# Kernel tuning notes

Measured on AMD Instinct MI355X. Metric: run time of the kernel, lower is better.

## Reference

```python
import jax, jax.numpy as jnp
import numpy as np

N = 16384
F_IN = 256
F_OUT = 256


def setup_inputs() -> dict:
    key = jax.random.key(0)
    k1, k2, k3 = jax.random.split(key, 3)
    x = jax.random.normal(k1, (N, F_IN), dtype=jnp.float32)
    # dense 0/1 adjacency (original masks with adj[j] == 1)
    adj = jax.random.randint(k2, (N, N), 0, 2, dtype=jnp.int32)
    # glorot-uniform init for weight [2F_in, F_out]
    stdv = np.sqrt(6.0 / (2 * F_IN + F_OUT)).astype(np.float32)
    weight = jax.random.uniform(k3, (2 * F_IN, F_OUT), dtype=jnp.float32,
                                minval=-stdv, maxval=stdv)
    bias = jnp.zeros((F_OUT,), dtype=jnp.float32)
    return {"x": x, "adj": adj, "weight": weight, "bias": bias}


def reference(x, adj, weight, bias):
    # Mean over neighbors (adj row == 1): segment-mean expressed as a
    # normalized dense matmul -- equivalent to the per-row boolean-mask mean.
    a = adj.astype(x.dtype)                      # [N, N]
    deg = jnp.sum(a, axis=1, keepdims=True)      # [N, 1]
    x1 = (a @ x) / deg                           # [N, F] neighbor mean
    n_x = jnp.concatenate([x1, x], axis=1)       # [N, 2F]
    return n_x @ weight + bias                   # [N, F_out]
```

## Files before the change

kernel.cpp:

```cpp
#include <hip/hip_runtime.h>
#include <hip/hip_bf16.h>
#include <stdint.h>


typedef short bf16x8 __attribute__((ext_vector_type(8)));
typedef float f32x4  __attribute__((ext_vector_type(4)));

__device__ __forceinline__ uint32_t pack_bf16_rne(float lo, float hi) {
    uint32_t ul = __float_as_uint(lo);
    uint32_t uh = __float_as_uint(hi);
    ul = (ul + 0x7fffu + ((ul >> 16) & 1u)) >> 16;
    uh = (uh + 0x7fffu + ((uh >> 16) & 1u)) >> 16;
    return ul | (uh << 16);
}

__global__ __launch_bounds__(256) void k_transpose_w(const float* __restrict__ w,
                                                     uint16_t* __restrict__ wt) {
    int idx = blockIdx.x * 256 + threadIdx.x;
    int n = idx >> 8;
    int k = idx & 255;
    int row = (n < 256) ? k : (256 + k);
    int col = (n < 256) ? n : (n - 256);
    uint32_t u = __float_as_uint(w[row * 256 + col]);
    u = (u + 0x7fffu + ((u >> 16) & 1u)) >> 16;
    wt[idx] = (uint16_t)u;
}

__global__ __launch_bounds__(256) void k_small_gemm(const float* __restrict__ x,
                                                    const uint16_t* __restrict__ wt,
                                                    const float* __restrict__ bias,
                                                    uint16_t* __restrict__ yTt,
                                                    float* __restrict__ z) {
    __shared__ uint16_t As[128 * 32];
    __shared__ uint16_t Bs[128 * 32];

    const int t  = threadIdx.x;
    const int ct = blockIdx.x;
    const int rt = blockIdx.y;
    const int m0 = rt * 128;
    const int n0 = ct * 128;

    const int lane = t & 63, w = t >> 6;
    const int wr = w >> 1, wc = w & 1;
    const int l15 = lane & 15, quad = lane >> 4;

    f32x4 acc[4][4] = {};

    float4 a_reg[4];
    uint4  b_reg[2];

#pragma unroll
    for (int i = 0; i < 4; ++i) {
        int f4 = t + 256 * i, row = f4 >> 3, c4 = f4 & 7;
        a_reg[i] = *(const float4*)(x + (m0 + row) * 256 + c4 * 4);
    }
#pragma unroll
    for (int i = 0; i < 2; ++i) {
        int u4 = t + 256 * i, n_l = u4 >> 2, part = u4 & 3;
        b_reg[i] = *(const uint4*)(wt + (n0 + n_l) * 256 + part * 8);
    }

    for (int kk = 0; kk < 8; ++kk) {
        __syncthreads();
#pragma unroll
        for (int i = 0; i < 4; ++i) {
            int f4 = t + 256 * i, row = f4 >> 3, c4 = f4 & 7;
            uint2 p;
            p.x = pack_bf16_rne(a_reg[i].x, a_reg[i].y);
            p.y = pack_bf16_rne(a_reg[i].z, a_reg[i].w);
            *(uint2*)(As + row * 32 + c4 * 4) = p;
        }
#pragma unroll
        for (int i = 0; i < 2; ++i) {
            int u4 = t + 256 * i, n_l = u4 >> 2, part = u4 & 3;
            *(uint4*)(Bs + n_l * 32 + part * 8) = b_reg[i];
        }
        if (kk < 7) {
            int k0 = (kk + 1) * 32;
#pragma unroll
            for (int i = 0; i < 4; ++i) {
                int f4 = t + 256 * i, row = f4 >> 3, c4 = f4 & 7;
                a_reg[i] = *(const float4*)(x + (m0 + row) * 256 + k0 + c4 * 4);
            }
#pragma unroll
            for (int i = 0; i < 2; ++i) {
                int u4 = t + 256 * i, n_l = u4 >> 2, part = u4 & 3;
                b_reg[i] = *(const uint4*)(wt + (n0 + n_l) * 256 + k0 + part * 8);
            }
        }
        __syncthreads();

        bf16x8 a_frag[4], b_frag[4];
#pragma unroll
        for (int fr = 0; fr < 4; ++fr)
            a_frag[fr] = *(const bf16x8*)(As + (wr * 64 + fr * 16 + l15) * 32 + quad * 8);
#pragma unroll
        for (int fc = 0; fc < 4; ++fc)
            b_frag[fc] = *(const bf16x8*)(Bs + (wc * 64 + fc * 16 + l15) * 32 + quad * 8);
#pragma unroll
        for (int fr = 0; fr < 4; ++fr)
#pragma unroll
            for (int fc = 0; fc < 4; ++fc)
                acc[fr][fc] = __builtin_amdgcn_mfma_f32_16x16x32_bf16(
                    a_frag[fr], b_frag[fc], acc[fr][fc], 0, 0, 0);
    }

    if (ct < 2) {
#pragma unroll
        for (int fr = 0; fr < 4; ++fr) {
            int m_base = m0 + wr * 64 + fr * 16 + quad * 4;
#pragma unroll
            for (int fc = 0; fc < 4; ++fc) {
                int n_g = n0 + wc * 64 + fc * 16 + l15;
                uint2 pp;
                pp.x = pack_bf16_rne(acc[fr][fc][0], acc[fr][fc][1]);
                pp.y = pack_bf16_rne(acc[fr][fc][2], acc[fr][fc][3]);
                *(uint2*)(yTt + (size_t)(m_base >> 5) * 8192 + n_g * 32 + (m_base & 31)) = pp;
            }
        }
    } else {
#pragma unroll
        for (int fr = 0; fr < 4; ++fr) {
            int m_base = m0 + wr * 64 + fr * 16 + quad * 4;
#pragma unroll
            for (int fc = 0; fc < 4; ++fc) {
                int n_g = (n0 - 256) + wc * 64 + fc * 16 + l15;
                float bv = bias[n_g];
#pragma unroll
                for (int r = 0; r < 4; ++r)
                    z[(size_t)(m_base + r) * 256 + n_g] = acc[fr][fc][r] + bv;
            }
        }
    }
}

#define A_STRIDE 36
#define A_SZ (64 * A_STRIDE)
#define KITER 256

#define STEP(ARD, AWR, KK)                                                      \
  do {                                                                          \
    if ((KK) < KITER - 1) {                                \
      _Pragma("unroll") for (int fc = 0; fc < 4; ++fc)                          \
        bN[fc] = *(const bf16x8*)(pB + fc * 512);                               \
      pB += 8192;                                                               \
    }                                                                           \
    if ((KK) < KITER - 3) {                                   \
      aN = pa4[0]; pa4 += 8;                                                    \
    }                                                                           \
    if ((KK) < KITER - 1) {                           \
      degp += aQ0.x + aQ0.y + aQ0.z + aQ0.w;                                    \
      uint2 pv;                                                                 \
      pv.x = (uint32_t)(aQ0.x | (aQ0.y << 16)) * 0x3F80u;                       \
      pv.y = (uint32_t)(aQ0.z | (aQ0.w << 16)) * 0x3F80u;                       \
      *(uint2*)&As##AWR[a_lds] = pv;                                            \
    }                                                                           \
    {                                                                           \
      bf16x8 af[2];                                                             \
      _Pragma("unroll") for (int fr = 0; fr < 2; ++fr) {                        \
        int row = wr * 32 + fr * 16 + l15;                                      \
        af[fr] = *(const bf16x8*)(As##ARD + row * A_STRIDE + quad * 8);         \
      }                                                                         \
      _Pragma("unroll") for (int fr = 0; fr < 2; ++fr)                          \
        _Pragma("unroll") for (int fc = 0; fc < 4; ++fc)                        \
          acc[fr][fc] = __builtin_amdgcn_mfma_f32_16x16x32_bf16(                \
              af[fr], bC[fc], acc[fr][fc], 0, 0, 0);                            \
    }                                                                           \
    aQ0 = aQ1; aQ1 = aQ2; aQ2 = aN;                                             \
    _Pragma("unroll") for (int fc = 0; fc < 4; ++fc) bC[fc] = bN[fc];           \
    asm volatile("s_waitcnt lgkmcnt(0)\n\ts_barrier" ::: "memory");             \
  } while (0)

__global__ __launch_bounds__(512, 4) void k_big_gemm(const int* __restrict__ adj,
                                                     const uint16_t* __restrict__ yTt,
                                                     float* __restrict__ part,
                                                     int* __restrict__ degw) {
    __shared__ uint16_t As0[A_SZ], As1[A_SZ], As2[A_SZ];

    const int t = threadIdx.x;
    const int id   = blockIdx.x + (int)gridDim.x * blockIdx.y;
    const int xcd  = id & 7, slot = id >> 3;
    const int ky   = xcd >> 2;
    const int m0   = ((xcd & 3) * 64 + slot) * 64;
    const int lane = t & 63, w = t >> 6;
    const int wr = w >> 2, wc = w & 3;
    const int l15 = lane & 15, quad = lane >> 4;

    f32x4 acc[2][4] = {};

    const int a_n = t >> 3, a_c4 = t & 7;
    const int4* pa4 = (const int4*)(adj + (size_t)(m0 + a_n) * 16384 + ky * 8192) + a_c4;
    const int a_lds = a_n * A_STRIDE + a_c4 * 4;

    const uint16_t* pB = yTt + (size_t)(ky * 256) * 8192
                       + (size_t)(wc * 64 + l15) * 32 + quad * 8;

    bf16x8 bC[4], bN[4];
    int4 aQ0, aQ1, aQ2, aN;
    int degp;

    int4 a0 = pa4[0];
    aQ0 = pa4[8];
    aQ1 = pa4[16];
    aQ2 = aQ1;
    aN  = aQ1;
    pa4 += 24;
#pragma unroll
    for (int fc = 0; fc < 4; ++fc) bN[fc] = *(const bf16x8*)(pB + fc * 512);
    pB += 8192;
#pragma unroll
    for (int fc = 0; fc < 4; ++fc) bC[fc] = bN[fc];

    degp = a0.x + a0.y + a0.z + a0.w;
    {
        uint2 pv;
        pv.x = (uint32_t)(a0.x | (a0.y << 16)) * 0x3F80u;
        pv.y = (uint32_t)(a0.z | (a0.w << 16)) * 0x3F80u;
        *(uint2*)&As0[a_lds] = pv;
    }
    asm volatile("s_waitcnt lgkmcnt(0)\n\ts_barrier" ::: "memory");

    for (int kk = 0; kk < KITER - 4; kk += 3) {
        STEP(0, 1, kk);
        STEP(1, 2, kk + 1);
        STEP(2, 0, kk + 2);
    }
    STEP(0, 1, 252);
    STEP(1, 2, 253);
    STEP(2, 0, 254);
    STEP(0, 1, 255);

    degp += __shfl_down(degp, 4);
    degp += __shfl_down(degp, 2);
    degp += __shfl_down(degp, 1);
    if ((t & 7) == 0) degw[ky * 16384 + m0 + a_n] = degp;

    float* pc = part + (size_t)ky * 16384 * 256;
#pragma unroll
    for (int fr = 0; fr < 2; ++fr) {
#pragma unroll
        for (int r = 0; r < 4; ++r) {
            int m_l = wr * 32 + fr * 16 + quad * 4 + r;
            size_t mrow = (size_t)(m0 + m_l) * 256;
#pragma unroll
            for (int fc = 0; fc < 4; ++fc) {
                int n_g = wc * 64 + fc * 16 + l15;
                pc[mrow + n_g] = acc[fr][fc][r];
            }
        }
    }
}

__global__ __launch_bounds__(256) void k_reduce(const float* __restrict__ part,
                                                const int* __restrict__ degw,
                                                const float* __restrict__ z,
                                                float* __restrict__ out) {
    int i4 = blockIdx.x * 256 + threadIdx.x;
    int m = i4 >> 6;
    float4 p0 = ((const float4*)part)[i4];
    float4 p1 = ((const float4*)part)[i4 + 16384 * 64];
    float4 zz = ((const float4*)z)[i4];
    float inv = 1.0f / (float)(degw[m] + degw[16384 + m]);
    float4 o;
    o.x = (p0.x + p1.x) * inv + zz.x;
    o.y = (p0.y + p1.y) * inv + zz.y;
    o.z = (p0.z + p1.z) * inv + zz.z;
    o.w = (p0.w + p1.w) * inv + zz.w;
    ((float4*)out)[i4] = o;
}

extern "C" void kernel_launch(void* const* d_in, const int* in_sizes, int n_in,
                              void* d_out, int out_size, void* d_ws, size_t ws_size,
                              hipStream_t stream) {
    const float* x      = (const float*)d_in[0];
    const int*   adj    = (const int*)d_in[1];
    const float* weight = (const float*)d_in[2];
    const float* bias   = (const float*)d_in[3];
    float* out = (float*)d_out;

    char* wsb = (char*)d_ws;
    uint16_t* wt   = (uint16_t*)(wsb);
    uint16_t* yTt  = (uint16_t*)(wsb + 262144);
    float*    z    = (float*)(wsb + 262144 + 8388608);
    float*    partb= (float*)(wsb + 262144 + 8388608 + 16777216);
    int*      degw = (int*)(wsb + 262144 + 8388608 + 16777216 + 33554432);

    k_transpose_w<<<512, 256, 0, stream>>>(weight, wt);
    k_small_gemm<<<dim3(4, 128), 256, 0, stream>>>(x, wt, bias, yTt, z);
    k_big_gemm<<<dim3(256, 2), 512, 0, stream>>>(adj, yTt, partb, degw);
    k_reduce<<<4096, 256, 0, stream>>>(partb, degw, z, out);
}
```

Measured before the change: 1.494 ms.

## Stage B tiles via direct global-to-LDS loads and split K three ways

The big adjacency GEMM now loads the yT operand straight into LDS with global_load_lds and reads it back through XOR-swizzled fragments, replacing per-thread register prefetch. The K split grows from 2 to 3 (171/171/170 tiles), giving 768 blocks, and the XCD-aware block remapping is dropped. The triple-buffered A staging becomes double-buffered, and the kernel adds nontemporal loads and stores, s_setprio around the MFMAs, and a higher occupancy hint. The reduce kernel now sums three partials and degree counts, which costs an extra 16MB partial write and read.

```diff
diff --git a/kernel.cpp b/kernel.cpp
--- a/kernel.cpp
+++ b/kernel.cpp
@@ -5,6 +5,7 @@
 
 typedef short bf16x8 __attribute__((ext_vector_type(8)));
 typedef float f32x4  __attribute__((ext_vector_type(4)));
+typedef int   i32x4  __attribute__((ext_vector_type(4)));
 
 __device__ __forceinline__ uint32_t pack_bf16_rne(float lo, float hi) {
     uint32_t ul = __float_as_uint(lo);
@@ -12,6 +13,12 @@
     ul = (ul + 0x7fffu + ((ul >> 16) & 1u)) >> 16;
     uh = (uh + 0x7fffu + ((uh >> 16) & 1u)) >> 16;
     return ul | (uh << 16);
+}
+
+__device__ __forceinline__ void gld_lds16(const uint16_t* g, uint16_t* l) {
+    __builtin_amdgcn_global_load_lds(
+        (const __attribute__((address_space(1))) void*)g,
+        (__attribute__((address_space(3))) void*)l, 16, 0, 0);
 }
 
 __global__ __launch_bounds__(256) void k_transpose_w(const float* __restrict__ w,
@@ -134,106 +141,109 @@
     }
 }
 
-#define A_STRIDE 36
-#define A_SZ (64 * A_STRIDE)
-#define KITER 256
-
-#define STEP(ARD, AWR, KK)                                                      \
+#define STEP(RD, WR, KK)                                                        \
   do {                                                                          \
-    if ((KK) < KITER - 1) {                                \
-      _Pragma("unroll") for (int fc = 0; fc < 4; ++fc)                          \
-        bN[fc] = *(const bf16x8*)(pB + fc * 512);                               \
-      pB += 8192;                                                               \
+    if ((KK) < ns - 1) {                                       \
+      gld_lds16(gB0, &Bs[WR][ldsB0]);                                           \
+      gld_lds16(gB1, &Bs[WR][ldsB1]);                                           \
+      gB0 += 8192; gB1 += 8192;                                                 \
     }                                                                           \
-    if ((KK) < KITER - 3) {                                   \
-      aN = pa4[0]; pa4 += 8;                                                    \
+    if ((KK) < ns - 2) {                        \
+      aN = __builtin_nontemporal_load(pa4); pa4 += 8;                           \
     }                                                                           \
-    if ((KK) < KITER - 1) {                           \
-      degp += aQ0.x + aQ0.y + aQ0.z + aQ0.w;                                    \
+    if ((KK) < ns - 1) {                                     \
+      degp += q1.x + q1.y + q1.z + q1.w;                                        \
       uint2 pv;                                                                 \
-      pv.x = (uint32_t)(aQ0.x | (aQ0.y << 16)) * 0x3F80u;                       \
-      pv.y = (uint32_t)(aQ0.z | (aQ0.w << 16)) * 0x3F80u;                       \
-      *(uint2*)&As##AWR[a_lds] = pv;                                            \
+      pv.x = (uint32_t)(q1.x | (q1.y << 16)) * 0x3F80u;                         \
+      pv.y = (uint32_t)(q1.z | (q1.w << 16)) * 0x3F80u;                         \
+      *(uint2*)&As[WR][a_wr] = pv;                                              \
     }                                                                           \
     {                                                                           \
       bf16x8 af[2];                                                             \
-      _Pragma("unroll") for (int fr = 0; fr < 2; ++fr) {                        \
-        int row = wr * 32 + fr * 16 + l15;                                      \
-        af[fr] = *(const bf16x8*)(As##ARD + row * A_STRIDE + quad * 8);         \
+      _Pragma("unroll") for (int fr = 0; fr < 2; ++fr)                          \
+        af[fr] = *(const bf16x8*)&As[RD][af_base + fr * 512];                   \
+      _Pragma("unroll") for (int fh = 0; fh < 2; ++fh) {                        \
+        bf16x8 bfr[2];                                                          \
+        _Pragma("unroll") for (int fc = 0; fc < 2; ++fc)                        \
+          bfr[fc] = *(const bf16x8*)&Bs[RD][bf_base + (fh * 2 + fc) * 512];     \
+        __builtin_amdgcn_s_setprio(1);                                          \
+        _Pragma("unroll") for (int fr = 0; fr < 2; ++fr)                        \
+          _Pragma("unroll") for (int fc = 0; fc < 2; ++fc)                      \
+            acc[fr][fh * 2 + fc] = __builtin_amdgcn_mfma_f32_16x16x32_bf16(     \
+                af[fr], bfr[fc], acc[fr][fh * 2 + fc], 0, 0, 0);                \
+        __builtin_amdgcn_s_setprio(0);                                          \
       }                                                                         \
-      _Pragma("unroll") for (int fr = 0; fr < 2; ++fr)                          \
-        _Pragma("unroll") for (int fc = 0; fc < 4; ++fc)                        \
-          acc[fr][fc] = __builtin_amdgcn_mfma_f32_16x16x32_bf16(                \
-              af[fr], bC[fc], acc[fr][fc], 0, 0, 0);                            \
     }                                                                           \
-    aQ0 = aQ1; aQ1 = aQ2; aQ2 = aN;                                             \
-    _Pragma("unroll") for (int fc = 0; fc < 4; ++fc) bC[fc] = bN[fc];           \
-    asm volatile("s_waitcnt lgkmcnt(0)\n\ts_barrier" ::: "memory");             \
+    q1 = aN;                                                                    \
+    if ((KK) < ns - 2)                                                          \
+      asm volatile("s_waitcnt vmcnt(1) lgkmcnt(0)\n\ts_barrier" ::: "memory");  \
+    else                                                                        \
+      asm volatile("s_waitcnt vmcnt(0) lgkmcnt(0)\n\ts_barrier" ::: "memory");  \
   } while (0)
 
-__global__ __launch_bounds__(512, 4) void k_big_gemm(const int* __restrict__ adj,
+__global__ __launch_bounds__(512, 6) void k_big_gemm(const int* __restrict__ adj,
                                                      const uint16_t* __restrict__ yTt,
                                                      float* __restrict__ part,
                                                      int* __restrict__ degw) {
-    __shared__ uint16_t As0[A_SZ], As1[A_SZ], As2[A_SZ];
+    __shared__ __align__(16) uint16_t As[2][64 * 32];
+    __shared__ __align__(16) uint16_t Bs[2][256 * 32];
 
     const int t = threadIdx.x;
-    const int id   = blockIdx.x + (int)gridDim.x * blockIdx.y;
-    const int xcd  = id & 7, slot = id >> 3;
-    const int ky   = xcd >> 2;
-    const int m0   = ((xcd & 3) * 64 + slot) * 64;
+    const int m0 = blockIdx.x * 64;
+    const int ky = blockIdx.y;
+    const int ns = (ky == 2) ? 170 : 171;
     const int lane = t & 63, w = t >> 6;
     const int wr = w >> 2, wc = w & 3;
     const int l15 = lane & 15, quad = lane >> 4;
+    const int xorq = quad ^ ((l15 >> 1) & 3);
 
     f32x4 acc[2][4] = {};
 
-    const int a_n = t >> 3, a_c4 = t & 7;
-    const int4* pa4 = (const int4*)(adj + (size_t)(m0 + a_n) * 16384 + ky * 8192) + a_c4;
-    const int a_lds = a_n * A_STRIDE + a_c4 * 4;
-
-    const uint16_t* pB = yTt + (size_t)(ky * 256) * 8192
-                       + (size_t)(wc * 64 + l15) * 32 + quad * 8;
-
-    bf16x8 bC[4], bN[4];
-    int4 aQ0, aQ1, aQ2, aN;
+    const int a_row = t >> 3, a_c4 = t & 7;
+    const i32x4* pa4 = (const i32x4*)(adj + (size_t)(m0 + a_row) * 16384 + ky * 5472) + a_c4;
+    const int a_wr = a_row * 32 + (((a_c4 >> 1) ^ ((a_row >> 1) & 3)) * 8) + (a_c4 & 1) * 4;
+
+    const int c0 = t, c1 = t + 512;
+    const size_t tile0 = (size_t)ky * 171;
+    const uint16_t* gB0 = yTt + tile0 * 8192
+        + (c0 >> 2) * 32 + (((c0 & 3) ^ ((c0 >> 3) & 3)) * 8);
+    const uint16_t* gB1 = yTt + tile0 * 8192
+        + (c1 >> 2) * 32 + (((c1 & 3) ^ ((c1 >> 3) & 3)) * 8);
+    const int ldsB0 = w * 512;
+    const int ldsB1 = w * 512 + 4096;
+
+    const int af_base = (wr * 32 + l15) * 32 + xorq * 8;
+    const int bf_base = (wc * 64 + l15) * 32 + xorq * 8;
+
+    i32x4 q1, aN;
     int degp;
 
-    int4 a0 = pa4[0];
-    aQ0 = pa4[8];
-    aQ1 = pa4[16];
-    aQ2 = aQ1;
-    aN  = aQ1;
-    pa4 += 24;
-#pragma unroll
-    for (int fc = 0; fc < 4; ++fc) bN[fc] = *(const bf16x8*)(pB + fc * 512);
-    pB += 8192;
-#pragma unroll
-    for (int fc = 0; fc < 4; ++fc) bC[fc] = bN[fc];
-
+    gld_lds16(gB0, &Bs[0][ldsB0]);
+    gld_lds16(gB1, &Bs[0][ldsB1]);
+    gB0 += 8192; gB1 += 8192;
+    i32x4 a0 = __builtin_nontemporal_load(pa4); pa4 += 8;
+    q1 = __builtin_nontemporal_load(pa4); pa4 += 8;
+    aN = q1;
     degp = a0.x + a0.y + a0.z + a0.w;
     {
         uint2 pv;
         pv.x = (uint32_t)(a0.x | (a0.y << 16)) * 0x3F80u;
         pv.y = (uint32_t)(a0.z | (a0.w << 16)) * 0x3F80u;
-        *(uint2*)&As0[a_lds] = pv;
-    }
-    asm volatile("s_waitcnt lgkmcnt(0)\n\ts_barrier" ::: "memory");
-
-    for (int kk = 0; kk < KITER - 4; kk += 3) {
+        *(uint2*)&As[0][a_wr] = pv;
+    }
+    asm volatile("s_waitcnt vmcnt(1) lgkmcnt(0)\n\ts_barrier" ::: "memory");
+
+    int kk = 0;
+    for (; kk + 1 < ns; kk += 2) {
         STEP(0, 1, kk);
-        STEP(1, 2, kk + 1);
-        STEP(2, 0, kk + 2);
-    }
-    STEP(0, 1, 252);
-    STEP(1, 2, 253);
-    STEP(2, 0, 254);
-    STEP(0, 1, 255);
+        STEP(1, 0, kk + 1);
+    }
+    if (kk < ns) STEP(0, 1, kk);
 
     degp += __shfl_down(degp, 4);
     degp += __shfl_down(degp, 2);
     degp += __shfl_down(degp, 1);
-    if ((t & 7) == 0) degw[ky * 16384 + m0 + a_n] = degp;
+    if ((t & 7) == 0) degw[ky * 16384 + m0 + a_row] = degp;
 
     float* pc = part + (size_t)ky * 16384 * 256;
 #pragma unroll
@@ -245,7 +255,7 @@
 #pragma unroll
             for (int fc = 0; fc < 4; ++fc) {
                 int n_g = wc * 64 + fc * 16 + l15;
-                pc[mrow + n_g] = acc[fr][fc][r];
+                __builtin_nontemporal_store(acc[fr][fc][r], &pc[mrow + n_g]);
             }
         }
     }
@@ -259,13 +269,14 @@
     int m = i4 >> 6;
     float4 p0 = ((const float4*)part)[i4];
     float4 p1 = ((const float4*)part)[i4 + 16384 * 64];
+    float4 p2 = ((const float4*)part)[i4 + 2 * 16384 * 64];
     float4 zz = ((const float4*)z)[i4];
-    float inv = 1.0f / (float)(degw[m] + degw[16384 + m]);
+    float inv = 1.0f / (float)(degw[m] + degw[16384 + m] + degw[32768 + m]);
     float4 o;
-    o.x = (p0.x + p1.x) * inv + zz.x;
-    o.y = (p0.y + p1.y) * inv + zz.y;
-    o.z = (p0.z + p1.z) * inv + zz.z;
-    o.w = (p0.w + p1.w) * inv + zz.w;
+    o.x = (p0.x + p1.x + p2.x) * inv + zz.x;
+    o.y = (p0.y + p1.y + p2.y) * inv + zz.y;
+    o.z = (p0.z + p1.z + p2.z) * inv + zz.z;
+    o.w = (p0.w + p1.w + p2.w) * inv + zz.w;
     ((float4*)out)[i4] = o;
 }
 
@@ -283,10 +294,10 @@
     uint16_t* yTt  = (uint16_t*)(wsb + 262144);
     float*    z    = (float*)(wsb + 262144 + 8388608);
     float*    partb= (float*)(wsb + 262144 + 8388608 + 16777216);
-    int*      degw = (int*)(wsb + 262144 + 8388608 + 16777216 + 33554432);
+    int*      degw = (int*)(wsb + 262144 + 8388608 + 16777216 + 50331648);
 
     k_transpose_w<<<512, 256, 0, stream>>>(weight, wt);
     k_small_gemm<<<dim3(4, 128), 256, 0, stream>>>(x, wt, bias, yTt, z);
-    k_big_gemm<<<dim3(256, 2), 512, 0, stream>>>(adj, yTt, partb, degw);
+    k_big_gemm<<<dim3(256, 3), 512, 0, stream>>>(adj, yTt, partb, degw);
     k_reduce<<<4096, 256, 0, stream>>>(partb, degw, z, out);
 }
```

Result: faster. 1.449 ms (-3.0%).
